# Performance work log

Measured on AMD Instinct MI355X. Metric: run time of the kernel, lower is better.

The kernel has to match this reference:

```python
import jax, jax.numpy as jnp
import numpy as np

B, T, C, K = 8, 4096, 256, 4  # batch, time, d_embd, k_periods


def setup_inputs() -> dict:
    key = jax.random.key(0)
    ks = jax.random.split(key, 5)
    x = jax.random.normal(ks[0], (B, T, C), jnp.float32)
    # inception stand-in: masked 3x3 conv (HWIO) + GELU
    Wc = jax.random.normal(ks[1], (3, 3, C, C), jnp.float32) * 0.02
    bc = jnp.zeros((C,), jnp.float32)
    # FeedForward params
    W1 = jax.random.normal(ks[2], (C, 4 * C), jnp.float32) * 0.02
    b1 = jnp.zeros((4 * C,), jnp.float32)
    W2 = jax.random.normal(ks[3], (4 * C, C), jnp.float32) * 0.02
    b2 = jnp.zeros((C,), jnp.float32)
    return {"x": x, "Wc": Wc, "bc": bc, "W1": W1, "b1": b1, "W2": W2, "b2": b2}


def _topk_freq_idx(x):
    # eager (concrete) period detection; shapes downstream are data-dependent,
    # exactly like the torch original (which is also not compilable as one graph)
    xf = jnp.fft.rfft(x, axis=1)[:, 1:, :]            # drop DC -> [B, T//2, C]
    amps_full = jnp.mean(jnp.abs(xf), axis=-1)        # [B, T//2]
    _, idx = jax.lax.top_k(amps_full, K)              # [B, K] indices into sliced bins
    return np.asarray(jax.device_get(idx))


def _fold(x, n):
    # vectorized per-sample 1D->2D folding with period n[b]; returns masked grid
    pad = (T - T % n) % n
    m = (T + pad) // n
    M, N = int(m.max()), int(n.max())
    nj = jnp.asarray(n)[:, None, None]                # [B,1,1]
    i = jnp.arange(M)[None, :, None]
    j = jnp.arange(N)[None, None, :]
    t = i * nj + j                                    # [B,M,N] flat time index
    valid = (j < nj) & (t < T)
    tc = jnp.clip(t, 0, T - 1)
    grid = x[jnp.arange(B)[:, None, None], tc] * valid[..., None]  # [B,M,N,C]
    mask = valid[..., None].astype(x.dtype)
    return grid, mask


def _inception(grid, mask, Wc, bc):
    y = jax.lax.conv_general_dilated(
        grid, Wc, window_strides=(1, 1), padding='SAME',
        dimension_numbers=('NHWC', 'HWIO', 'NHWC'))
    return jax.nn.gelu(y + bc, approximate=False) * mask


def _unfold(y, n):
    ts = jnp.arange(T)[None, :]
    nj = jnp.asarray(n)[:, None]
    return y[jnp.arange(B)[:, None], ts // nj, ts % nj]  # [B,T,C]


def _forward(x, Wc, bc, W1, b1, W2, b2, idx_np):
    # differentiable amplitude recomputation with fixed (closed-over) indices
    xf = jnp.fft.rfft(x, axis=1)[:, 1:, :]
    amps_full = jnp.mean(jnp.abs(xf), axis=-1)                     # [B, T//2]
    amps_k = jnp.take_along_axis(amps_full, jnp.asarray(idx_np), axis=1)  # [B,K]
    # original computes p = T // topk_index; clamp to avoid div-by-zero on idx 0
    p = np.maximum(T // np.maximum(idx_np, 1), 1)                   # [B,K] np ints
    outs = []
    for k in range(K):
        grid, mask = _fold(x, p[:, k])
        y = _inception(grid, mask, Wc, bc)
        outs.append(_unfold(y, p[:, k]))
    tf = jnp.stack(outs, axis=1)                                   # [B,K,T,C]
    h = jax.nn.gelu(tf @ W1 + b1, approximate=False) @ W2 + b2     # FeedForward
    w = jax.nn.softmax(amps_k, axis=-1)[:, :, None, None]
    return x + (h * w).sum(axis=1)


def reference(x, Wc, bc, W1, b1, W2, b2):
    idx_np = _topk_freq_idx(x)
    return _forward(x, Wc, bc, W1, b1, W2, b2, idx_np)
```

## Files before the change

kernel.cpp:

```cpp
#include <hip/hip_runtime.h>
#include <cstdint>
#include <cstddef>

#define T_LEN 4096
#define C_DIM 256
#define B_DIM 8
#define K_TOP 4

typedef __attribute__((ext_vector_type(8))) short bf16x8;
typedef __attribute__((ext_vector_type(4))) float f32x4;

__device__ __forceinline__ float gelu_fast(float x) {
    float x2 = x * x;
    float a = x * fmaf(0.071354816f, x2, 1.595769122f);
    float e = __expf(-a);
    return __fdividef(x, 1.0f + e);
}

__device__ __forceinline__ unsigned short f2bf(float f) {
    uint32_t u = __float_as_uint(f);
    uint32_t r = (u + 0x7fffu + ((u >> 16) & 1u)) >> 16;
    return (unsigned short)r;
}

typedef __attribute__((address_space(3))) uint32_t lds_u32_t;
typedef __attribute__((address_space(1))) const uint32_t gbl_u32_t;

__device__ __forceinline__ void lds_load16(const void* g, void* l) {
    __builtin_amdgcn_global_load_lds((gbl_u32_t*)g, (lds_u32_t*)l, 16, 0, 0);
}

#define BAR_VM0()                                                      \
    do {                                                               \
        asm volatile("s_waitcnt vmcnt(0) lgkmcnt(0)" ::: "memory");    \
        __builtin_amdgcn_s_barrier();                                  \
        __builtin_amdgcn_sched_barrier(0);                             \
    } while (0)
#define BAR_VM3()                                                      \
    do {                                                               \
        asm volatile("s_waitcnt vmcnt(3) lgkmcnt(0)" ::: "memory");    \
        __builtin_amdgcn_s_barrier();                                  \
        __builtin_amdgcn_sched_barrier(0);                             \
    } while (0)
#define BAR_LGKM()                                                     \
    do {                                                               \
        asm volatile("s_waitcnt lgkmcnt(0)" ::: "memory");             \
        __builtin_amdgcn_s_barrier();                                  \
        __builtin_amdgcn_sched_barrier(0);                             \
    } while (0)

#define FPAD(i) ((i) + ((i) >> 5))

__global__ __launch_bounds__(256) void cvt_x_kernel(const float4* __restrict__ x,
                                                    float4* __restrict__ out,
                                                    ushort4* __restrict__ xbf,
                                                    unsigned short* __restrict__ zbuf) {
    size_t i = (size_t)blockIdx.x * 256 + threadIdx.x;
    float4 v = x[i];
    out[i] = v;
    ushort4 o;
    o.x = f2bf(v.x); o.y = f2bf(v.y); o.z = f2bf(v.z); o.w = f2bf(v.w);
    xbf[i] = o;
    if (blockIdx.x == 0 && threadIdx.x < 256) zbuf[threadIdx.x] = 0;
}

__global__ __launch_bounds__(256) void transpose_cvt_kernel(const float* __restrict__ src,
                                                            unsigned short* __restrict__ dst,
                                                            int R, int C) {
    __shared__ float t[32][33];
    const int c0 = blockIdx.x * 32, r0 = blockIdx.y * 32;
    const int lx = threadIdx.x & 31, ly = threadIdx.x >> 5;
    for (int rr = ly; rr < 32; rr += 8) {
        int r = r0 + rr, c = c0 + lx;
        t[rr][lx] = (r < R && c < C) ? src[(size_t)r * C + c] : 0.0f;
    }
    __syncthreads();
    for (int rr = ly; rr < 32; rr += 8) {
        int c = c0 + rr, r = r0 + lx;
        if (r < R && c < C) dst[(size_t)c * R + r] = f2bf(t[lx][rr]);
    }
}

__global__ __launch_bounds__(256) void repack_frag_kernel(const float* __restrict__ src,
                                                          unsigned short* __restrict__ dst,
                                                          int K, int N) {
    int idx = blockIdx.x * 256 + threadIdx.x;
    int total = (N >> 4) * (K >> 5) * 64;
    if (idx >= total) return;
    int lane = idx & 63, tile = idx >> 6;
    int ktiles = K >> 5;
    int tile_n = tile / ktiles, tile_k = tile % ktiles;
    int col = tile_n * 16 + (lane & 15);
    int k0 = tile_k * 32 + (lane >> 4) * 8;
    __align__(16) unsigned short v[8];
#pragma unroll
    for (int j = 0; j < 8; j++) v[j] = f2bf(src[(size_t)(k0 + j) * N + col]);
    *(uint4*)(dst + (size_t)idx * 8) = *(const uint4*)v;
}

__global__ __launch_bounds__(256) void transpose_x_kernel(const float* __restrict__ x,
                                                          float* __restrict__ xT) {
    __shared__ float tile[32][33];
    const int b = blockIdx.z;
    const int t0 = blockIdx.x * 32, c0 = blockIdx.y * 32;
    const int lx = threadIdx.x & 31, ly = threadIdx.x >> 5;
    const float* xp = x + (size_t)b * T_LEN * C_DIM;
    float* op = xT + (size_t)b * C_DIM * T_LEN;
    for (int rr = ly; rr < 32; rr += 8)
        tile[rr][lx] = xp[(size_t)(t0 + rr) * C_DIM + c0 + lx];
    __syncthreads();
    for (int rr = ly; rr < 32; rr += 8)
        op[(size_t)(c0 + rr) * T_LEN + t0 + lx] = tile[lx][rr];
}

__global__ __launch_bounds__(256) void fft_mag_kernel(const float* __restrict__ src,
                                                      float* __restrict__ mags,
                                                      int transposed) {
    const int bx = blockIdx.x;
    const int b = bx >> 8;
    const int c = bx & 255;
    const int tid = threadIdx.x;

    __shared__ __align__(16) float re[4224];
    __shared__ __align__(16) float im[4224];
    __shared__ __align__(16) float twr[2048];
    __shared__ __align__(16) float twi[2048];

    for (int u = tid; u < 2048; u += 256) {
        float ang = -6.283185307179586f * (float)u / 4096.0f;
        float s, co;
        sincosf(ang, &s, &co);
        twr[u] = co;
        twi[u] = s;
    }
    for (int i = tid; i < 4224; i += 256) im[i] = 0.0f;

    if (transposed) {
        const float4* row = (const float4*)(src + ((size_t)(b * C_DIM + c)) * T_LEN);
        for (int e4 = tid; e4 < 1024; e4 += 256) {
            float4 v = row[e4];
            int e = e4 * 4;
            re[FPAD((int)(__brev((unsigned)(e + 0)) >> 20))] = v.x;
            re[FPAD((int)(__brev((unsigned)(e + 1)) >> 20))] = v.y;
            re[FPAD((int)(__brev((unsigned)(e + 2)) >> 20))] = v.z;
            re[FPAD((int)(__brev((unsigned)(e + 3)) >> 20))] = v.w;
        }
    } else {
        const float* xp = src + (size_t)b * T_LEN * C_DIM + c;
        for (int e = tid; e < 4096; e += 256) {
            int r = (int)(__brev((unsigned)e) >> 20);
            re[FPAD(r)] = xp[(size_t)e * C_DIM];
        }
    }
    __syncthreads();

#pragma unroll
    for (int sp = 0; sp < 6; sp++) {
        const int h = 1 << (2 * sp);
        const int t1s = 11 - 2 * sp;
        const int t2s = 10 - 2 * sp;
        for (int j = tid; j < 1024; j += 256) {
            int p = j & (h - 1);
            int G = j >> (2 * sp);
            int base = G * 4 * h + p;
            int iA = FPAD(base), iB = FPAD(base + h);
            int iC = FPAD(base + 2 * h), iD = FPAD(base + 3 * h);
            float w1r = twr[p << t1s], w1i = twi[p << t1s];
            float w2r = twr[p << t2s], w2i = twi[p << t2s];
            float Ar = re[iA], Ai = im[iA], Br = re[iB], Bi = im[iB];
            float Cr = re[iC], Ci = im[iC], Dr = re[iD], Di = im[iD];
            float tBr = w1r * Br - w1i * Bi, tBi = w1r * Bi + w1i * Br;
            float tDr = w1r * Dr - w1i * Di, tDi = w1r * Di + w1i * Dr;
            float A1r = Ar + tBr, A1i = Ai + tBi;
            float B1r = Ar - tBr, B1i = Ai - tBi;
            float C1r = Cr + tDr, C1i = Ci + tDi;
            float D1r = Cr - tDr, D1i = Ci - tDi;
            float tCr = w2r * C1r - w2i * C1i, tCi = w2r * C1i + w2i * C1r;
            float uDr = w2r * D1r - w2i * D1i, uDi = w2r * D1i + w2i * D1r;
            float vDr = uDi, vDi = -uDr;
            re[iA] = A1r + tCr; im[iA] = A1i + tCi;
            re[iC] = A1r - tCr; im[iC] = A1i - tCi;
            re[iB] = B1r + vDr; im[iB] = B1i + vDi;
            re[iD] = B1r - vDr; im[iD] = B1i - vDi;
        }
        __syncthreads();
    }

    float* mp = mags + ((size_t)(b * C_DIM + c)) * 2048;
    for (int u = tid; u < 2048; u += 256) {
        int f = FPAD(u + 1);
        mp[u] = sqrtf(re[f] * re[f] + im[f] * im[f]);
    }
}

__global__ __launch_bounds__(256) void reduce_amps_kernel(const float* __restrict__ mags,
                                                          float* __restrict__ partial) {
    const int b = blockIdx.z, cc = blockIdx.y;
    const int u = blockIdx.x * 256 + threadIdx.x;
    const float* mp = mags + ((size_t)b * C_DIM + cc * 32) * 2048 + u;
    float s = 0.0f;
    for (int c = 0; c < 32; c++) s += mp[(size_t)c * 2048];
    partial[((size_t)b * 8 + cc) * 2048 + u] = s;
}

__global__ __launch_bounds__(256) void topk_kernel(const float* __restrict__ partial,
                                                   int* __restrict__ meta_p,
                                                   float* __restrict__ meta_w) {
    const int b = blockIdx.x;
    const int tid = threadIdx.x;
    __shared__ float v[2048];
    __shared__ float rv[256];
    __shared__ int ri[256];
    __shared__ float topv[K_TOP];
    __shared__ int topi[K_TOP];

    for (int u = tid; u < 2048; u += 256) {
        float s = 0.0f;
        for (int cc = 0; cc < 8; cc++) s += partial[((size_t)b * 8 + cc) * 2048 + u];
        v[u] = s * (1.0f / (float)C_DIM);
    }

    for (int k = 0; k < K_TOP; k++) {
        __syncthreads();
        float bv = -1e30f;
        int bi = 2048;
        for (int u = tid; u < 2048; u += 256) {
            float val = v[u];
            if (val > bv) { bv = val; bi = u; }
        }
        rv[tid] = bv;
        ri[tid] = bi;
        __syncthreads();
        for (int s = 128; s > 0; s >>= 1) {
            if (tid < s) {
                float ov = rv[tid + s];
                int oi = ri[tid + s];
                if (ov > rv[tid] || (ov == rv[tid] && oi < ri[tid])) {
                    rv[tid] = ov;
                    ri[tid] = oi;
                }
            }
            __syncthreads();
        }
        if (tid == 0) {
            topv[k] = rv[0];
            topi[k] = ri[0];
            v[ri[0]] = -1e30f;
        }
    }
    __syncthreads();
    if (tid == 0) {
        float mx = topv[0];
        for (int k = 1; k < K_TOP; k++) mx = fmaxf(mx, topv[k]);
        float e[K_TOP], se = 0.0f;
        for (int k = 0; k < K_TOP; k++) { e[k] = expf(topv[k] - mx); se += e[k]; }
        for (int k = 0; k < K_TOP; k++) {
            int idx = topi[k];
            int d = (idx >= 1) ? idx : 1;
            int p = T_LEN / d;
            if (p < 1) p = 1;
            meta_p[b * K_TOP + k] = p;
            meta_w[b * K_TOP + k] = e[k] / se;
        }
    }
}

__global__ __launch_bounds__(512) void conv_mfma_kernel(const unsigned short* __restrict__ xbf,
                                                        const unsigned short* __restrict__ WcT,
                                                        const float* __restrict__ bc,
                                                        const int* __restrict__ meta_p,
                                                        const unsigned short* __restrict__ zbuf,
                                                        unsigned short* __restrict__ convbufs,
                                                        size_t conv_stride, int koff) {
    const int b = blockIdx.y;
    const int kz = blockIdx.z;
    const int n = meta_p[b * K_TOP + koff + kz];
    const int row0 = blockIdx.x * 128;
    const int tid = threadIdx.x, w = tid >> 6, lane = tid & 63;
    const int wm = w >> 2, wn = w & 3;

    __shared__ __align__(16) unsigned short Al[3][128 * 32];
    __shared__ __align__(16) unsigned short Bl[3][256 * 32];

    const int ra = tid >> 2;
    const int swz = ((tid & 3) ^ ((ra >> 1) & 3)) * 8;
    int ti, tj;
    {
        int t = row0 + ra;
        ti = t / n;
        tj = t - ti * n;
    }
    const unsigned short* xb = xbf + (size_t)b * T_LEN * C_DIM;
    const unsigned short* baseB0 = WcT + (size_t)ra * 2304 + swz;
    const unsigned short* baseB1 = WcT + (size_t)(ra + 128) * 2304 + swz;

    auto computeA = [&](int q) -> const unsigned short* {
        int di = q / 3 - 1, dj = q % 3 - 1;
        int ii = ti + di, jj = tj + dj;
        int tp = ii * n + jj;
        bool ok = (jj >= 0) && (jj < n) && (ii >= 0) && (tp < T_LEN);
        return ok ? (xb + (size_t)tp * C_DIM + swz) : (zbuf + swz);
    };

    f32x4 acc[4][4];
#pragma unroll
    for (int m = 0; m < 4; m++)
#pragma unroll
        for (int nn = 0; nn < 4; nn++) acc[m][nn] = (f32x4){0.f, 0.f, 0.f, 0.f};

    const unsigned short* baseA = computeA(0);
    lds_load16(baseA, &Al[0][tid * 8]);
    lds_load16(baseB0, &Bl[0][tid * 8]);
    lds_load16(baseB1, &Bl[0][4096 + tid * 8]);
    lds_load16(baseA + 32, &Al[1][tid * 8]);
    lds_load16(baseB0 + 32, &Bl[1][tid * 8]);
    lds_load16(baseB1 + 32, &Bl[1][4096 + tid * 8]);

    int cur = 0, stb = 2;
    for (int s = 0; s < 72; s++) {
        if (s < 71) BAR_VM3();
        else        BAR_VM0();

        const int t = s + 2;
        if (t < 72) {
            if ((t & 7) == 0) baseA = computeA(t >> 3);
            lds_load16(baseA + (t & 7) * 32, &Al[stb][tid * 8]);
            lds_load16(baseB0 + (size_t)t * 32, &Bl[stb][tid * 8]);
            lds_load16(baseB1 + (size_t)t * 32, &Bl[stb][4096 + tid * 8]);
        }

        bf16x8 af[4], bfr[4];
#pragma unroll
        for (int m = 0; m < 4; m++) {
            int row = wm * 64 + m * 16 + (lane & 15);
            af[m] = *(const bf16x8*)((const char*)&Al[cur][0] + row * 64 +
                                     (((lane >> 4) * 16) ^ (((row >> 1) & 3) << 4)));
        }
#pragma unroll
        for (int nn = 0; nn < 4; nn++) {
            int rowb = wn * 64 + nn * 16 + (lane & 15);
            bfr[nn] = *(const bf16x8*)((const char*)&Bl[cur][0] + rowb * 64 +
                                       (((lane >> 4) * 16) ^ (((rowb >> 1) & 3) << 4)));
        }
        __builtin_amdgcn_s_setprio(1);
#pragma unroll
        for (int m = 0; m < 4; m++)
#pragma unroll
            for (int nn = 0; nn < 4; nn++)
                acc[m][nn] = __builtin_amdgcn_mfma_f32_16x16x32_bf16(af[m], bfr[nn], acc[m][nn], 0, 0, 0);
        __builtin_amdgcn_s_setprio(0);

        cur = (cur == 2) ? 0 : cur + 1;
        stb = (stb == 2) ? 0 : stb + 1;
    }

    unsigned short* ob = convbufs + (size_t)kz * conv_stride + (size_t)b * T_LEN * C_DIM;
#pragma unroll
    for (int nn = 0; nn < 4; nn++) {
        int col = wn * 64 + nn * 16 + (lane & 15);
        float bs = bc[col];
#pragma unroll
        for (int m = 0; m < 4; m++) {
            int rbase = row0 + wm * 64 + m * 16 + (lane >> 4) * 4;
#pragma unroll
            for (int r = 0; r < 4; r++) {
                float v = acc[m][nn][r] + bs;
                ob[(size_t)(rbase + r) * C_DIM + col] = f2bf(gelu_fast(v));
            }
        }
    }
}

__global__ __launch_bounds__(256, 2) void fused_ff_kernel(
    const unsigned short* __restrict__ convbufs, size_t conv_stride,
    const unsigned short* __restrict__ W1frag,
    const unsigned short* __restrict__ W2frag,
    const float* __restrict__ b1,
    const float* __restrict__ b2,
    const float* __restrict__ meta_w,
    float* __restrict__ out,
    int koff, int kcount) {
    const int tid = threadIdx.x;
    const int wn = tid >> 6, lane = tid & 63;
    const int row0 = blockIdx.x * 64;
    const int b = row0 >> 12;

    __shared__ __align__(16) unsigned short Asw[64 * 256];
    __shared__ __align__(16) unsigned short Hsw[2][64 * 128];
    __shared__ __align__(16) float b1s[1024];

    auto stageA = [&](const unsigned short* Ag) {
#pragma unroll
        for (int u = 0; u < 8; u++) {
            int ch = u * 256 + tid;
            int row = ch >> 5;
            int cole = ((ch & 31) * 8) ^ ((row & 7) << 3);
            lds_load16(Ag + (size_t)row * 256 + cole, (unsigned short*)Asw + (size_t)ch * 8);
        }
    };

    for (int i = tid; i < 1024; i += 256) b1s[i] = b1[i];

    f32x4 acc2[4][4];
#pragma unroll
    for (int m = 0; m < 4; m++)
#pragma unroll
        for (int nn = 0; nn < 4; nn++) acc2[m][nn] = (f32x4){0.f, 0.f, 0.f, 0.f};

    stageA(convbufs + (size_t)row0 * C_DIM);

    for (int kk = koff; kk < koff + kcount; kk++) {
        BAR_VM0();
        const float wk = meta_w[b * K_TOP + kk];

        for (int cc = 0; cc < 8; cc++) {
            const int par = cc & 1;
            f32x4 acc1[2][4];
#pragma unroll
            for (int n2 = 0; n2 < 2; n2++)
#pragma unroll
                for (int t4 = 0; t4 < 4; t4++) acc1[n2][t4] = (f32x4){0.f, 0.f, 0.f, 0.f};

            __builtin_amdgcn_s_setprio(1);
#pragma unroll
            for (int ks = 0; ks < 8; ks++) {
                bf16x8 bfA[4], w1f[2];
#pragma unroll
                for (int t4 = 0; t4 < 4; t4++) {
                    int row = t4 * 16 + (lane & 15);
                    bfA[t4] = *(const bf16x8*)((const char*)Asw + row * 512 +
                                               ((ks * 64 + (lane >> 4) * 16) ^ ((row & 7) << 4)));
                }
#pragma unroll
                for (int n2 = 0; n2 < 2; n2++) {
                    int tile_n = cc * 8 + wn * 2 + n2;
                    w1f[n2] = *(const bf16x8*)(W1frag + ((size_t)(tile_n * 8 + ks) * 64 + lane) * 8);
                }
#pragma unroll
                for (int n2 = 0; n2 < 2; n2++)
#pragma unroll
                    for (int t4 = 0; t4 < 4; t4++)
                        acc1[n2][t4] = __builtin_amdgcn_mfma_f32_16x16x32_bf16(w1f[n2], bfA[t4],
                                                                               acc1[n2][t4], 0, 0, 0);
            }
            __builtin_amdgcn_s_setprio(0);

#pragma unroll
            for (int n2 = 0; n2 < 2; n2++) {
                const int hb = wn * 32 + n2 * 16 + (lane >> 4) * 4;
                f32x4 bb4 = *(const f32x4*)&b1s[cc * 128 + hb];
#pragma unroll
                for (int t4 = 0; t4 < 4; t4++) {
                    int t = t4 * 16 + (lane & 15);
                    float g0 = wk * gelu_fast(acc1[n2][t4][0] + bb4[0]);
                    float g1 = wk * gelu_fast(acc1[n2][t4][1] + bb4[1]);
                    float g2 = wk * gelu_fast(acc1[n2][t4][2] + bb4[2]);
                    float g3 = wk * gelu_fast(acc1[n2][t4][3] + bb4[3]);
                    uint32_t lo, hi;
                    asm("v_cvt_pk_bf16_f32 %0, %1, %2" : "=v"(lo) : "v"(g0), "v"(g1));
                    asm("v_cvt_pk_bf16_f32 %0, %1, %2" : "=v"(hi) : "v"(g2), "v"(g3));
                    uint2 pk;
                    pk.x = lo;
                    pk.y = hi;
                    *(uint2*)((char*)&Hsw[par][0] + t * 256 +
                              ((hb * 2) ^ ((t & 7) << 4))) = pk;
                }
            }
            BAR_LGKM();

            if (cc == 7 && kk + 1 < koff + kcount)
                stageA(convbufs + (size_t)(kk + 1 - koff) * conv_stride + (size_t)row0 * C_DIM);

            __builtin_amdgcn_s_setprio(1);
#pragma unroll
            for (int ks2 = 0; ks2 < 4; ks2++) {
                bf16x8 af2[4], bf2[4];
#pragma unroll
                for (int m = 0; m < 4; m++) {
                    int row = m * 16 + (lane & 15);
                    af2[m] = *(const bf16x8*)((const char*)&Hsw[par][0] + row * 256 +
                                              ((ks2 * 64 + (lane >> 4) * 16) ^ ((row & 7) << 4)));
                }
#pragma unroll
                for (int nn = 0; nn < 4; nn++) {
                    int tile_n = wn * 4 + nn;
                    int tile_k = cc * 4 + ks2;
                    bf2[nn] = *(const bf16x8*)(W2frag + ((size_t)(tile_n * 32 + tile_k) * 64 + lane) * 8);
                }
#pragma unroll
                for (int m = 0; m < 4; m++)
#pragma unroll
                    for (int nn = 0; nn < 4; nn++)
                        acc2[m][nn] = __builtin_amdgcn_mfma_f32_16x16x32_bf16(af2[m], bf2[nn],
                                                                              acc2[m][nn], 0, 0, 0);
            }
            __builtin_amdgcn_s_setprio(0);
        }
    }

#pragma unroll
    for (int nn = 0; nn < 4; nn++) {
        int col = wn * 64 + nn * 16 + (lane & 15);
        float bb = b2[col];
#pragma unroll
        for (int m = 0; m < 4; m++) {
            int rbase = row0 + m * 16 + (lane >> 4) * 4;
#pragma unroll
            for (int r = 0; r < 4; r++)
                out[(size_t)(rbase + r) * C_DIM + col] += acc2[m][nn][r] + bb;
        }
    }
}

extern "C" void kernel_launch(void* const* d_in, const int* in_sizes, int n_in,
                              void* d_out, int out_size, void* d_ws, size_t ws_size,
                              hipStream_t stream) {
    const float* x  = (const float*)d_in[0];
    const float* Wc = (const float*)d_in[1];
    const float* bc = (const float*)d_in[2];
    const float* W1 = (const float*)d_in[3];
    const float* b1 = (const float*)d_in[4];
    const float* W2 = (const float*)d_in[5];
    const float* b2 = (const float*)d_in[6];
    float* out = (float*)d_out;

    const size_t CONV_ELEMS = (size_t)B_DIM * T_LEN * C_DIM;
    const size_t CONV_BYTES = CONV_ELEMS * 2;
    const size_t MAGS_BYTES = (size_t)B_DIM * C_DIM * 2048 * 4;
    const size_t XT_BYTES = (size_t)B_DIM * T_LEN * C_DIM * 4;

    uint8_t* ws = (uint8_t*)d_ws;
    size_t off = 0;
    auto alloc = [&](size_t bytes) {
        size_t o = off;
        off = (off + bytes + 255) & ~(size_t)255;
        return o;
    };
    float* partial = (float*)(ws + alloc((size_t)B_DIM * 8 * 2048 * 4));
    int* meta_p = (int*)(ws + alloc(B_DIM * K_TOP * 4));
    float* meta_w = (float*)(ws + alloc(B_DIM * K_TOP * 4));
    unsigned short* xbf = (unsigned short*)(ws + alloc((size_t)B_DIM * T_LEN * C_DIM * 2));
    unsigned short* WcT = (unsigned short*)(ws + alloc((size_t)256 * 2304 * 2));
    unsigned short* W1frag = (unsigned short*)(ws + alloc((size_t)256 * 1024 * 2));
    unsigned short* W2frag = (unsigned short*)(ws + alloc((size_t)1024 * 256 * 2));
    unsigned short* zbuf = (unsigned short*)(ws + alloc(512));

    size_t remaining = (ws_size > off) ? (ws_size - off) : 0;
    uint8_t* regionA = ws + off;
    int tier;
    if (remaining >= 4 * CONV_BYTES) tier = 2;
    else if (remaining >= MAGS_BYTES + XT_BYTES) tier = 1;
    else tier = 0;

    float* mags = (float*)regionA;
    float* xT = (float*)(regionA + ((tier == 2) ? CONV_BYTES : MAGS_BYTES));
    unsigned short* convbufs = (unsigned short*)regionA;
    const int use_xT = (tier >= 1);

    cvt_x_kernel<<<dim3((B_DIM * T_LEN * C_DIM / 4) / 256), 256, 0, stream>>>(
        (const float4*)x, (float4*)out, (ushort4*)xbf, zbuf);

    transpose_cvt_kernel<<<dim3(256 / 32, 2304 / 32), 256, 0, stream>>>(Wc, WcT, 2304, 256);
    repack_frag_kernel<<<dim3(128), 256, 0, stream>>>(W1, W1frag, 256, 1024);
    repack_frag_kernel<<<dim3(128), 256, 0, stream>>>(W2, W2frag, 1024, 256);

    if (use_xT) {
        transpose_x_kernel<<<dim3(T_LEN / 32, C_DIM / 32, B_DIM), 256, 0, stream>>>(x, xT);
        fft_mag_kernel<<<dim3(B_DIM * C_DIM), 256, 0, stream>>>(xT, mags, 1);
    } else {
        fft_mag_kernel<<<dim3(B_DIM * C_DIM), 256, 0, stream>>>(x, mags, 0);
    }
    reduce_amps_kernel<<<dim3(2048 / 256, 8, B_DIM), 256, 0, stream>>>(mags, partial);
    topk_kernel<<<dim3(B_DIM), 256, 0, stream>>>(partial, meta_p, meta_w);

    if (tier == 2) {
        conv_mfma_kernel<<<dim3(32, B_DIM, K_TOP), 512, 0, stream>>>(
            xbf, WcT, bc, meta_p, zbuf, convbufs, CONV_ELEMS, 0);
        fused_ff_kernel<<<dim3(B_DIM * T_LEN / 64), 256, 0, stream>>>(
            convbufs, CONV_ELEMS, W1frag, W2frag, b1, b2, meta_w, out, 0, K_TOP);
    } else {
        for (int k = 0; k < K_TOP; k++) {
            conv_mfma_kernel<<<dim3(32, B_DIM, 1), 512, 0, stream>>>(
                xbf, WcT, bc, meta_p, zbuf, convbufs, 0, k);
            fused_ff_kernel<<<dim3(B_DIM * T_LEN / 64), 256, 0, stream>>>(
                convbufs, 0, W1frag, W2frag, b1, b2, meta_w, out, k, 1);
        }
    }
}
```

Before: 445.3 us.

## Sum gelu-weighted hidden across periods before a single second FF GEMM

```diff
diff --git a/kernel.cpp b/kernel.cpp
--- a/kernel.cpp
+++ b/kernel.cpp
@@ -52,12 +52,10 @@
 #define FPAD(i) ((i) + ((i) >> 5))
 
 __global__ __launch_bounds__(256) void cvt_x_kernel(const float4* __restrict__ x,
-                                                    float4* __restrict__ out,
                                                     ushort4* __restrict__ xbf,
                                                     unsigned short* __restrict__ zbuf) {
     size_t i = (size_t)blockIdx.x * 256 + threadIdx.x;
     float4 v = x[i];
-    out[i] = v;
     ushort4 o;
     o.x = f2bf(v.x); o.y = f2bf(v.y); o.z = f2bf(v.z); o.w = f2bf(v.w);
     xbf[i] = o;
@@ -371,6 +369,7 @@
     }
 }
 
+template <int KCNT>
 __global__ __launch_bounds__(256, 2) void fused_ff_kernel(
     const unsigned short* __restrict__ convbufs, size_t conv_stride,
     const unsigned short* __restrict__ W1frag,
@@ -379,135 +378,148 @@
     const float* __restrict__ b2,
     const float* __restrict__ meta_w,
     float* __restrict__ out,
-    int koff, int kcount) {
+    const float* __restrict__ osrc,
+    float b2scale, int koff) {
     const int tid = threadIdx.x;
     const int wn = tid >> 6, lane = tid & 63;
-    const int row0 = blockIdx.x * 64;
+    const int row0 = blockIdx.x * 32;
     const int b = row0 >> 12;
 
-    __shared__ __align__(16) unsigned short Asw[64 * 256];
-    __shared__ __align__(16) unsigned short Hsw[2][64 * 128];
-    __shared__ __align__(16) float b1s[1024];
-
-    auto stageA = [&](const unsigned short* Ag) {
-#pragma unroll
-        for (int u = 0; u < 8; u++) {
+    __shared__ __align__(16) unsigned short Asw[KCNT * 32 * 256];
+    __shared__ __align__(16) unsigned short Hsw[2][32 * 128];
+
+    float wkv[KCNT];
+#pragma unroll
+    for (int kc = 0; kc < KCNT; kc++) wkv[kc] = meta_w[b * K_TOP + koff + kc];
+
+    {
+        const unsigned short* base = convbufs + (size_t)row0 * C_DIM;
+#pragma unroll
+        for (int u = 0; u < KCNT * 4; u++) {
             int ch = u * 256 + tid;
-            int row = ch >> 5;
-            int cole = ((ch & 31) * 8) ^ ((row & 7) << 3);
-            lds_load16(Ag + (size_t)row * 256 + cole, (unsigned short*)Asw + (size_t)ch * 8);
-        }
-    };
-
-    for (int i = tid; i < 1024; i += 256) b1s[i] = b1[i];
-
-    f32x4 acc2[4][4];
-#pragma unroll
-    for (int m = 0; m < 4; m++)
-#pragma unroll
-        for (int nn = 0; nn < 4; nn++) acc2[m][nn] = (f32x4){0.f, 0.f, 0.f, 0.f};
-
-    stageA(convbufs + (size_t)row0 * C_DIM);
-
-    for (int kk = koff; kk < koff + kcount; kk++) {
-        BAR_VM0();
-        const float wk = meta_w[b * K_TOP + kk];
-
-        for (int cc = 0; cc < 8; cc++) {
-            const int par = cc & 1;
-            f32x4 acc1[2][4];
+            int rfull = ch >> 5;
+            int kc = rfull >> 5;
+            int trow = rfull & 31;
+            int cole = ((ch & 31) * 8) ^ ((rfull & 7) << 3);
+            lds_load16(base + (size_t)kc * conv_stride + (size_t)trow * 256 + cole,
+                       (unsigned short*)Asw + (size_t)ch * 8);
+        }
+    }
+
+    f32x4 acc2[2][4];
+#pragma unroll
+    for (int t2 = 0; t2 < 2; t2++)
+#pragma unroll
+        for (int nn = 0; nn < 4; nn++) acc2[t2][nn] = (f32x4){0.f, 0.f, 0.f, 0.f};
+
+    BAR_VM0();
+
+    for (int cc = 0; cc < 8; cc++) {
+        const int par = cc & 1;
+
+        f32x4 acc1[KCNT][2][2];
+#pragma unroll
+        for (int kc = 0; kc < KCNT; kc++)
 #pragma unroll
             for (int n2 = 0; n2 < 2; n2++)
 #pragma unroll
-                for (int t4 = 0; t4 < 4; t4++) acc1[n2][t4] = (f32x4){0.f, 0.f, 0.f, 0.f};
-
-            __builtin_amdgcn_s_setprio(1);
-#pragma unroll
-            for (int ks = 0; ks < 8; ks++) {
-                bf16x8 bfA[4], w1f[2];
-#pragma unroll
-                for (int t4 = 0; t4 < 4; t4++) {
-                    int row = t4 * 16 + (lane & 15);
-                    bfA[t4] = *(const bf16x8*)((const char*)Asw + row * 512 +
-                                               ((ks * 64 + (lane >> 4) * 16) ^ ((row & 7) << 4)));
+                for (int t2 = 0; t2 < 2; t2++) acc1[kc][n2][t2] = (f32x4){0.f, 0.f, 0.f, 0.f};
+
+        __builtin_amdgcn_s_setprio(1);
+#pragma unroll
+        for (int ks = 0; ks < 8; ks++) {
+            bf16x8 w1f[2];
+#pragma unroll
+            for (int n2 = 0; n2 < 2; n2++) {
+                int tile_n = cc * 8 + wn * 2 + n2;
+                w1f[n2] = *(const bf16x8*)(W1frag + ((size_t)(tile_n * 8 + ks) * 64 + lane) * 8);
+            }
+            bf16x8 af[KCNT][2];
+#pragma unroll
+            for (int kc = 0; kc < KCNT; kc++)
+#pragma unroll
+                for (int t2 = 0; t2 < 2; t2++) {
+                    int row = kc * 32 + t2 * 16 + (lane & 15);
+                    af[kc][t2] = *(const bf16x8*)((const char*)Asw + row * 512 +
+                                                  ((ks * 64 + (lane >> 4) * 16) ^ ((row & 7) << 4)));
                 }
 #pragma unroll
-                for (int n2 = 0; n2 < 2; n2++) {
-                    int tile_n = cc * 8 + wn * 2 + n2;
-                    w1f[n2] = *(const bf16x8*)(W1frag + ((size_t)(tile_n * 8 + ks) * 64 + lane) * 8);
+            for (int kc = 0; kc < KCNT; kc++)
+#pragma unroll
+                for (int n2 = 0; n2 < 2; n2++)
+#pragma unroll
+                    for (int t2 = 0; t2 < 2; t2++)
+                        acc1[kc][n2][t2] = __builtin_amdgcn_mfma_f32_16x16x32_bf16(
+                            w1f[n2], af[kc][t2], acc1[kc][n2][t2], 0, 0, 0);
+        }
+        __builtin_amdgcn_s_setprio(0);
+
+#pragma unroll
+        for (int n2 = 0; n2 < 2; n2++) {
+            const int hloc = wn * 32 + n2 * 16 + (lane >> 4) * 4;
+            f32x4 bb = *(const f32x4*)(b1 + cc * 128 + hloc);
+#pragma unroll
+            for (int t2 = 0; t2 < 2; t2++) {
+                float hc[4];
+#pragma unroll
+                for (int r = 0; r < 4; r++) {
+                    float s = 0.0f;
+#pragma unroll
+                    for (int kc = 0; kc < KCNT; kc++)
+                        s += wkv[kc] * gelu_fast(acc1[kc][n2][t2][r] + bb[r]);
+                    hc[r] = s;
                 }
-#pragma unroll
-                for (int n2 = 0; n2 < 2; n2++)
-#pragma unroll
-                    for (int t4 = 0; t4 < 4; t4++)
-                        acc1[n2][t4] = __builtin_amdgcn_mfma_f32_16x16x32_bf16(w1f[n2], bfA[t4],
-                                                                               acc1[n2][t4], 0, 0, 0);
+                uint32_t lo, hi;
+                asm("v_cvt_pk_bf16_f32 %0, %1, %2" : "=v"(lo) : "v"(hc[0]), "v"(hc[1]));
+                asm("v_cvt_pk_bf16_f32 %0, %1, %2" : "=v"(hi) : "v"(hc[2]), "v"(hc[3]));
+                uint2 pk;
+                pk.x = lo;
+                pk.y = hi;
+                int t = t2 * 16 + (lane & 15);
+                *(uint2*)((char*)&Hsw[par][0] + t * 256 +
+                          ((hloc * 2) ^ ((t & 7) << 4))) = pk;
             }
-            __builtin_amdgcn_s_setprio(0);
-
-#pragma unroll
-            for (int n2 = 0; n2 < 2; n2++) {
-                const int hb = wn * 32 + n2 * 16 + (lane >> 4) * 4;
-                f32x4 bb4 = *(const f32x4*)&b1s[cc * 128 + hb];
-#pragma unroll
-                for (int t4 = 0; t4 < 4; t4++) {
-                    int t = t4 * 16 + (lane & 15);
-                    float g0 = wk * gelu_fast(acc1[n2][t4][0] + bb4[0]);
-                    float g1 = wk * gelu_fast(acc1[n2][t4][1] + bb4[1]);
-                    float g2 = wk * gelu_fast(acc1[n2][t4][2] + bb4[2]);
-                    float g3 = wk * gelu_fast(acc1[n2][t4][3] + bb4[3]);
-                    uint32_t lo, hi;
-                    asm("v_cvt_pk_bf16_f32 %0, %1, %2" : "=v"(lo) : "v"(g0), "v"(g1));
-                    asm("v_cvt_pk_bf16_f32 %0, %1, %2" : "=v"(hi) : "v"(g2), "v"(g3));
-                    uint2 pk;
-                    pk.x = lo;
-                    pk.y = hi;
-                    *(uint2*)((char*)&Hsw[par][0] + t * 256 +
-                              ((hb * 2) ^ ((t & 7) << 4))) = pk;
-                }
+        }
+        BAR_LGKM();
+
+        __builtin_amdgcn_s_setprio(1);
+#pragma unroll
+        for (int ks2 = 0; ks2 < 4; ks2++) {
+            bf16x8 af2[2], w2f[4];
+#pragma unroll
+            for (int t2 = 0; t2 < 2; t2++) {
+                int row = t2 * 16 + (lane & 15);
+                af2[t2] = *(const bf16x8*)((const char*)&Hsw[par][0] + row * 256 +
+                                           ((ks2 * 64 + (lane >> 4) * 16) ^ ((row & 7) << 4)));
             }
-            BAR_LGKM();
-
-            if (cc == 7 && kk + 1 < koff + kcount)
-                stageA(convbufs + (size_t)(kk + 1 - koff) * conv_stride + (size_t)row0 * C_DIM);
-
-            __builtin_amdgcn_s_setprio(1);
-#pragma unroll
-            for (int ks2 = 0; ks2 < 4; ks2++) {
-                bf16x8 af2[4], bf2[4];
-#pragma unroll
-                for (int m = 0; m < 4; m++) {
-                    int row = m * 16 + (lane & 15);
-                    af2[m] = *(const bf16x8*)((const char*)&Hsw[par][0] + row * 256 +
-                                              ((ks2 * 64 + (lane >> 4) * 16) ^ ((row & 7) << 4)));
-                }
-#pragma unroll
-                for (int nn = 0; nn < 4; nn++) {
-                    int tile_n = wn * 4 + nn;
-                    int tile_k = cc * 4 + ks2;
-                    bf2[nn] = *(const bf16x8*)(W2frag + ((size_t)(tile_n * 32 + tile_k) * 64 + lane) * 8);
-                }
-#pragma unroll
-                for (int m = 0; m < 4; m++)
-#pragma unroll
-                    for (int nn = 0; nn < 4; nn++)
-                        acc2[m][nn] = __builtin_amdgcn_mfma_f32_16x16x32_bf16(af2[m], bf2[nn],
-                                                                              acc2[m][nn], 0, 0, 0);
+#pragma unroll
+            for (int nn = 0; nn < 4; nn++) {
+                int tile_n = wn * 4 + nn;
+                int tile_k = cc * 4 + ks2;
+                w2f[nn] = *(const bf16x8*)(W2frag + ((size_t)(tile_n * 32 + tile_k) * 64 + lane) * 8);
             }
-            __builtin_amdgcn_s_setprio(0);
-        }
+#pragma unroll
+            for (int t2 = 0; t2 < 2; t2++)
+#pragma unroll
+                for (int nn = 0; nn < 4; nn++)
+                    acc2[t2][nn] = __builtin_amdgcn_mfma_f32_16x16x32_bf16(af2[t2], w2f[nn],
+                                                                           acc2[t2][nn], 0, 0, 0);
+        }
+        __builtin_amdgcn_s_setprio(0);
     }
 
 #pragma unroll
     for (int nn = 0; nn < 4; nn++) {
         int col = wn * 64 + nn * 16 + (lane & 15);
-        float bb = b2[col];
-#pragma unroll
-        for (int m = 0; m < 4; m++) {
-            int rbase = row0 + m * 16 + (lane >> 4) * 4;
-#pragma unroll
-            for (int r = 0; r < 4; r++)
-                out[(size_t)(rbase + r) * C_DIM + col] += acc2[m][nn][r] + bb;
+        float bb = b2scale * b2[col];
+#pragma unroll
+        for (int t2 = 0; t2 < 2; t2++) {
+            int rbase = row0 + t2 * 16 + (lane >> 4) * 4;
+#pragma unroll
+            for (int r = 0; r < 4; r++) {
+                size_t idx = (size_t)(rbase + r) * C_DIM + col;
+                out[idx] = osrc[idx] + acc2[t2][nn][r] + bb;
+            }
         }
     }
 }
@@ -558,7 +570,7 @@
     const int use_xT = (tier >= 1);
 
     cvt_x_kernel<<<dim3((B_DIM * T_LEN * C_DIM / 4) / 256), 256, 0, stream>>>(
-        (const float4*)x, (float4*)out, (ushort4*)xbf, zbuf);
+        (const float4*)x, (ushort4*)xbf, zbuf);
 
     transpose_cvt_kernel<<<dim3(256 / 32, 2304 / 32), 256, 0, stream>>>(Wc, WcT, 2304, 256);
     repack_frag_kernel<<<dim3(128), 256, 0, stream>>>(W1, W1frag, 256, 1024);
@@ -576,14 +588,15 @@
     if (tier == 2) {
         conv_mfma_kernel<<<dim3(32, B_DIM, K_TOP), 512, 0, stream>>>(
             xbf, WcT, bc, meta_p, zbuf, convbufs, CONV_ELEMS, 0);
-        fused_ff_kernel<<<dim3(B_DIM * T_LEN / 64), 256, 0, stream>>>(
-            convbufs, CONV_ELEMS, W1frag, W2frag, b1, b2, meta_w, out, 0, K_TOP);
+        fused_ff_kernel<4><<<dim3(B_DIM * T_LEN / 32), 256, 0, stream>>>(
+            convbufs, CONV_ELEMS, W1frag, W2frag, b1, b2, meta_w, out, x, 1.0f, 0);
     } else {
         for (int k = 0; k < K_TOP; k++) {
             conv_mfma_kernel<<<dim3(32, B_DIM, 1), 512, 0, stream>>>(
                 xbf, WcT, bc, meta_p, zbuf, convbufs, 0, k);
-            fused_ff_kernel<<<dim3(B_DIM * T_LEN / 64), 256, 0, stream>>>(
-                convbufs, 0, W1frag, W2frag, b1, b2, meta_w, out, k, 1);
-        }
-    }
-}
+            fused_ff_kernel<1><<<dim3(B_DIM * T_LEN / 32), 256, 0, stream>>>(
+                convbufs, 0, W1frag, W2frag, b1, b2, meta_w, out,
+                (k == 0) ? x : out, (k == K_TOP - 1) ? 1.0f : 0.0f, k);
+        }
+    }
+}
```

Result: faster. 392.0 us (-12.0%).
